# Optimization experiments

Hardware: AMD Instinct MI355X
Metric: run time of the kernel (lower is better)

The kernel has to match this reference:

```python
import jax, jax.numpy as jnp
import numpy as np

MAX_THRESHOLD = 0.25  # init kwarg
B, S, D, E = 8, 4096, 512, 8


def setup_inputs() -> dict:
    key = jax.random.key(0)
    ks = jax.random.split(key, 5)
    scale = 1.0 / np.sqrt(D)
    return {
        "inputs": jax.random.normal(ks[0], (B, S, D), dtype=jnp.float32),
        "W_gate": jax.random.normal(ks[1], (D, E), dtype=jnp.float32) * scale,
        "b_gate": jnp.zeros((E,), dtype=jnp.float32),
        "W_thr": jax.random.normal(ks[2], (D, 1), dtype=jnp.float32) * scale,
        "b_thr": jnp.zeros((1,), dtype=jnp.float32),
        "W_exp": jax.random.normal(ks[3], (E, D, D), dtype=jnp.float32) * scale,
        "b_exp": jnp.zeros((E, D), dtype=jnp.float32),
    }


def reference(inputs, W_gate, b_gate, W_thr, b_thr, W_exp, b_exp):
    d = inputs.shape[-1]
    x = inputs.reshape(-1, d)  # [T, D]
    # gating
    gate_logits = jax.nn.softmax(x @ W_gate + b_gate, axis=-1)          # [T, E]
    thresholds = jax.nn.sigmoid(x @ W_thr + b_thr) * MAX_THRESHOLD      # [T, 1]
    adapted = gate_logits - thresholds                                  # [T, E]
    selected = (adapted >= 0).astype(x.dtype)                           # [T, E]
    weights = adapted * selected                                        # [T, E]
    wsum = jnp.sum(weights, axis=-1, keepdims=True)
    wsum = jnp.where(wsum == 0, jnp.ones_like(wsum), wsum)
    weights = weights / wsum
    # dense-equivalent of gather->expert->scatter (weights are 0 where unselected)
    ex_out = jnp.einsum('td,edf->etf', x, W_exp) + b_exp[:, None, :]    # [E, T, D]
    results = jnp.einsum('etf,te->tf', ex_out, weights)                 # [T, D]
    return results.reshape(inputs.shape[:-1] + (results.shape[-1],))
```

## Files before the change

kernel.cpp:

```cpp
#include <hip/hip_runtime.h>


#define T_TOKENS 32768
#define DDIM 512
#define KDIM 4096
#define SLOTA 8192
#define SLOTB 16384

typedef __attribute__((ext_vector_type(8))) short short8;
typedef __attribute__((ext_vector_type(4))) float floatx4;
typedef __bf16 bf16x2 __attribute__((ext_vector_type(2)));

__device__ __forceinline__ unsigned short f2bf(float f) {
    unsigned int u = __float_as_uint(f);
    u += 0x7FFFu + ((u >> 16) & 1u);
    return (unsigned short)(u >> 16);
}

__device__ __forceinline__ unsigned int pk2(float a, float b) {
#if __has_builtin(__builtin_amdgcn_cvt_pk_bf16_f32)
    bf16x2 v = __builtin_amdgcn_cvt_pk_bf16_f32(a, b);
    return __builtin_bit_cast(unsigned int, v);
#else
    return (unsigned int)f2bf(a) | ((unsigned int)f2bf(b) << 16);
#endif
}

__device__ __forceinline__ void async_copy16(const void* g, void* l) {
    __builtin_amdgcn_global_load_lds(
        (const __attribute__((address_space(1))) void*)g,
        (__attribute__((address_space(3))) void*)l, 16, 0, 0);
}

__global__ __launch_bounds__(256) void gating_cvt(
    const float* __restrict__ x, const float* __restrict__ Wg,
    const float* __restrict__ bg, const float* __restrict__ Wt,
    const float* __restrict__ bt, float* __restrict__ wbuf,
    unsigned short* __restrict__ Xbf)
{
    __shared__ float sW[512 * 12];
    const int tid = threadIdx.x;
    for (int i = tid; i < 512 * 9; i += 256) {
        int d = i / 9, e = i - d * 9;
        sW[d * 12 + e] = (e < 8) ? Wg[d * 8 + e] : Wt[d];
    }
    __syncthreads();

    const int t = blockIdx.x * 64 + (tid >> 2);
    const int q = tid & 3;
    float g[9];
#pragma unroll
    for (int e = 0; e < 9; ++e) g[e] = 0.f;

    const float4* xr = (const float4*)(x + (size_t)t * 512 + q * 128);
    for (int i = 0; i < 32; ++i) {
        float4 v = xr[i];
        float xv[4] = {v.x, v.y, v.z, v.w};
        const float* wp = &sW[(q * 128 + i * 4) * 12];
#pragma unroll
        for (int c = 0; c < 4; ++c) {
            const float* w = wp + c * 12;
#pragma unroll
            for (int e = 0; e < 9; ++e) g[e] = fmaf(xv[c], w[e], g[e]);
        }
    }
#pragma unroll
    for (int e = 0; e < 9; ++e) {
        g[e] += __shfl_xor(g[e], 1);
        g[e] += __shfl_xor(g[e], 2);
    }
    if (q == 0) {
#pragma unroll
        for (int e = 0; e < 8; ++e) g[e] += bg[e];
        g[8] += bt[0];
        float m = g[0];
#pragma unroll
        for (int e = 1; e < 8; ++e) m = fmaxf(m, g[e]);
        float s = 0.f;
        float p[8];
#pragma unroll
        for (int e = 0; e < 8; ++e) { p[e] = __expf(g[e] - m); s += p[e]; }
        const float inv = 1.f / s;
        const float thr = 0.25f / (1.f + __expf(-g[8]));
        float w8[8];
        float ws = 0.f;
#pragma unroll
        for (int e = 0; e < 8; ++e) {
            float a = p[e] * inv - thr;
            w8[e] = a > 0.f ? a : 0.f;
            ws += w8[e];
        }
        if (ws == 0.f) ws = 1.f;
        const float invw = 1.f / ws;
        float4 o0, o1;
        o0.x = w8[0] * invw; o0.y = w8[1] * invw; o0.z = w8[2] * invw; o0.w = w8[3] * invw;
        o1.x = w8[4] * invw; o1.y = w8[5] * invw; o1.z = w8[6] * invw; o1.w = w8[7] * invw;
        float4* op = (float4*)(wbuf + (size_t)t * 8);
        op[0] = o0;
        op[1] = o1;
    }

    const size_t base = (size_t)blockIdx.x * 64 * 512;
    const float4* xs = (const float4*)(x + base);
    uint2* xd = (uint2*)(Xbf + base);
#pragma unroll 4
    for (int it = 0; it < 32; ++it) {
        float4 v = xs[it * 256 + tid];
        uint2 pk;
        pk.x = pk2(v.x, v.y);
        pk.y = pk2(v.z, v.w);
        xd[it * 256 + tid] = pk;
    }
}

__global__ __launch_bounds__(256) void build_bt(
    const float* __restrict__ Wexp, unsigned short* __restrict__ Bt)
{
    __shared__ float tile[64][65];
    const int k0 = blockIdx.x * 64;
    const int n0 = blockIdx.y * 64;
    const int tid = threadIdx.x;
    const int r = tid >> 4, cq = tid & 15;
#pragma unroll
    for (int p = 0; p < 4; ++p) {
        const int rr = p * 16 + r;
        const float4 v = *(const float4*)(Wexp + (size_t)(k0 + rr) * 512 + n0 + cq * 4);
        tile[rr][cq * 4 + 0] = v.x;
        tile[rr][cq * 4 + 1] = v.y;
        tile[rr][cq * 4 + 2] = v.z;
        tile[rr][cq * 4 + 3] = v.w;
    }
    __syncthreads();
    const int rn = tid >> 2;
    const int kq = tid & 3;
    alignas(16) unsigned short buf[16];
#pragma unroll
    for (int j = 0; j < 16; ++j) buf[j] = f2bf(tile[kq * 16 + j][rn]);
    unsigned short* dst = Bt + (size_t)(n0 + rn) * KDIM + k0 + kq * 16;
    *(uint4*)(dst) = *(const uint4*)(buf);
    *(uint4*)(dst + 8) = *(const uint4*)(buf + 8);
}

__global__ __launch_bounds__(512, 2) void moe_gemm(
    const unsigned short* __restrict__ Xbf, const float* __restrict__ wbuf,
    const float* __restrict__ bexp, const unsigned short* __restrict__ Bt,
    float* __restrict__ out)
{
    __shared__ alignas(16) unsigned short As[3 * 128 * 64];
    __shared__ alignas(16) unsigned short Bs[3 * 256 * 64];
    __shared__ float sWbT[8 * 128];

    const int tid = threadIdx.x;
    const int wave = tid >> 6;
    const int lane = tid & 63;
    const int wm = wave >> 2;
    const int wn = wave & 3;
    const int lm = lane & 15;
    const int lq = lane >> 4;
    const int brow = lane >> 3;
    const int cg = (lane & 7) ^ brow;

    const int lin = blockIdx.x;
    const int g = lin & 7;
    const int j_ = lin >> 3;
    const int t0 = (g * 32 + (j_ >> 1)) * 128;
    const int n0 = (j_ & 1) * 256;

    {
        const int row = tid & 127, q = tid >> 7;
        const float2 w2 = *(const float2*)(wbuf + (size_t)(t0 + row) * 8 + q * 2);
        sWbT[(q * 2 + 0) * 128 + row] = w2.x;
        sWbT[(q * 2 + 1) * 128 + row] = w2.y;
    }

#define STAGE(s_, slot_)                                                        \
    {                                                                           \
        const int d0_ = ((s_) & 7) << 6;                                        \
        _Pragma("unroll")                                                       \
        for (int i = 0; i < 2; ++i)                                             \
            async_copy16(Xbf + (size_t)(t0 + wave * 16 + i * 8 + brow) * 512 + d0_ + cg * 8, \
                         As + (slot_) * SLOTA + (wave * 16 + i * 8) * 64);      \
        const int k0_ = (s_) << 6;                                              \
        _Pragma("unroll")                                                       \
        for (int i = 0; i < 4; ++i)                                             \
            async_copy16(Bt + (size_t)(n0 + wave * 32 + i * 8 + brow) * KDIM + k0_ + cg * 8, \
                         Bs + (slot_) * SLOTB + (wave * 32 + i * 8) * 64);      \
    }

    STAGE(0, 0);
    STAGE(1, 1);
    __syncthreads();

    floatx4 acc[4][4], tmp[4][4];
#pragma unroll
    for (int i = 0; i < 4; ++i)
#pragma unroll
        for (int j = 0; j < 4; ++j) {
            acc[i][j] = (floatx4){0.f, 0.f, 0.f, 0.f};
            tmp[i][j] = (floatx4){0.f, 0.f, 0.f, 0.f};
        }

    int sl = 0;
    for (int s = 0; s < 64; ++s) {
        if (s < 62) {
            const int sl2 = (sl >= 1) ? sl - 1 : 2;
            STAGE(s + 2, sl2);
        }
        const unsigned short* Ab = As + sl * SLOTA;
        const unsigned short* Bb = Bs + sl * SLOTB;
        __builtin_amdgcn_s_setprio(1);
#pragma unroll
        for (int kk = 0; kk < 2; ++kk) {
            const int ch = kk * 4 + lq;
            short8 a[4], b[4];
#pragma unroll
            for (int i = 0; i < 4; ++i) {
                const int row = wm * 64 + i * 16 + lm;
                a[i] = *(const short8*)(Ab + row * 64 + ((ch ^ (row & 7)) << 3));
            }
#pragma unroll
            for (int j = 0; j < 4; ++j) {
                const int row = wn * 64 + j * 16 + lm;
                b[j] = *(const short8*)(Bb + row * 64 + ((ch ^ (row & 7)) << 3));
            }
#pragma unroll
            for (int i = 0; i < 4; ++i)
#pragma unroll
                for (int j = 0; j < 4; ++j)
                    tmp[i][j] = __builtin_amdgcn_mfma_f32_16x16x32_bf16(
                        a[i], b[j], tmp[i][j], 0, 0, 0);
        }
        __builtin_amdgcn_s_setprio(0);
        if ((s & 7) == 7) {
            const int e = s >> 3;
#pragma unroll
            for (int i = 0; i < 4; ++i) {
                const float4 wq = *(const float4*)(sWbT + e * 128 + wm * 64 + i * 16 + lq * 4);
#pragma unroll
                for (int j = 0; j < 4; ++j) {
                    acc[i][j][0] = fmaf(wq.x, tmp[i][j][0], acc[i][j][0]);
                    acc[i][j][1] = fmaf(wq.y, tmp[i][j][1], acc[i][j][1]);
                    acc[i][j][2] = fmaf(wq.z, tmp[i][j][2], acc[i][j][2]);
                    acc[i][j][3] = fmaf(wq.w, tmp[i][j][3], acc[i][j][3]);
                    tmp[i][j] = (floatx4){0.f, 0.f, 0.f, 0.f};
                }
            }
        }
        if (s < 62) {
            asm volatile("s_waitcnt vmcnt(6)" ::: "memory");
        } else if (s == 62) {
            asm volatile("s_waitcnt vmcnt(0)" ::: "memory");
        }
        if (s < 63) __builtin_amdgcn_s_barrier();
        sl = (sl >= 2) ? 0 : sl + 1;
    }

    float bc[4][8];
#pragma unroll
    for (int j = 0; j < 4; ++j) {
        const int col = n0 + wn * 64 + j * 16 + lm;
#pragma unroll
        for (int e = 0; e < 8; ++e) bc[j][e] = bexp[e * 512 + col];
    }
#pragma unroll
    for (int i = 0; i < 4; ++i)
#pragma unroll
        for (int r = 0; r < 4; ++r) {
            const int rowl = wm * 64 + i * 16 + lq * 4 + r;
            const float4 w0 = *(const float4*)(wbuf + (size_t)(t0 + rowl) * 8);
            const float4 w1 = *(const float4*)(wbuf + (size_t)(t0 + rowl) * 8 + 4);
            float* op = out + (size_t)(t0 + rowl) * 512 + n0 + wn * 64 + lm;
#pragma unroll
            for (int j = 0; j < 4; ++j) {
                float bias = w0.x * bc[j][0];
                bias = fmaf(w0.y, bc[j][1], bias);
                bias = fmaf(w0.z, bc[j][2], bias);
                bias = fmaf(w0.w, bc[j][3], bias);
                bias = fmaf(w1.x, bc[j][4], bias);
                bias = fmaf(w1.y, bc[j][5], bias);
                bias = fmaf(w1.z, bc[j][6], bias);
                bias = fmaf(w1.w, bc[j][7], bias);
                op[j * 16] = acc[i][j][r] + bias;
            }
        }
#undef STAGE
}

extern "C" void kernel_launch(void* const* d_in, const int* in_sizes, int n_in,
                              void* d_out, int out_size, void* d_ws, size_t ws_size,
                              hipStream_t stream) {
    const float* x   = (const float*)d_in[0];
    const float* Wg  = (const float*)d_in[1];
    const float* bg  = (const float*)d_in[2];
    const float* Wt  = (const float*)d_in[3];
    const float* bt  = (const float*)d_in[4];
    const float* Wex = (const float*)d_in[5];
    const float* bex = (const float*)d_in[6];
    float* out = (float*)d_out;

    unsigned short* Xbf = (unsigned short*)d_ws;
    unsigned short* Bt  = (unsigned short*)((char*)d_ws + (size_t)T_TOKENS * DDIM * 2);
    float* wbuf = (float*)((char*)d_ws + (size_t)T_TOKENS * DDIM * 2
                                       + (size_t)DDIM * KDIM * 2);

    gating_cvt<<<T_TOKENS / 64, 256, 0, stream>>>(x, Wg, bg, Wt, bt, wbuf, Xbf);
    build_bt<<<dim3(KDIM / 64, DDIM / 64), 256, 0, stream>>>(Wex, Bt);
    moe_gemm<<<512, 512, 0, stream>>>(Xbf, wbuf, bex, Bt, out);
}
```

Measured before the change: 322.1 us.

## Interleave async global loads with LDS reads and MFMA in two half-steps

Splits each K-step into two halves. Each half reads its A/B fragments from LDS, then issues part of the async prefetch for stage s+2 (A plus half of B first, the rest of B second), then runs the MFMA block between extra barriers. The goal is to spread global-load issue across the compute and keep waves in lockstep so memory and MFMA overlap better. It adds two more block-wide barriers per iteration, which may cost synchronisation stalls.

```diff
diff --git a/kernel.cpp b/kernel.cpp
--- a/kernel.cpp
+++ b/kernel.cpp
@@ -146,8 +146,8 @@
     const float* __restrict__ bexp, const unsigned short* __restrict__ Bt,
     float* __restrict__ out)
 {
-    __shared__ alignas(16) unsigned short As[3 * 128 * 64];
-    __shared__ alignas(16) unsigned short Bs[3 * 256 * 64];
+    __shared__ alignas(16) unsigned short As[3 * SLOTA];
+    __shared__ alignas(16) unsigned short Bs[3 * SLOTB];
     __shared__ float sWbT[8 * 128];
 
     const int tid = threadIdx.x;
@@ -173,22 +173,27 @@
         sWbT[(q * 2 + 1) * 128 + row] = w2.y;
     }
 
-#define STAGE(s_, slot_)                                                        \
+#define STAGE_A(s_, slot_)                                                      \
     {                                                                           \
         const int d0_ = ((s_) & 7) << 6;                                        \
         _Pragma("unroll")                                                       \
         for (int i = 0; i < 2; ++i)                                             \
             async_copy16(Xbf + (size_t)(t0 + wave * 16 + i * 8 + brow) * 512 + d0_ + cg * 8, \
                          As + (slot_) * SLOTA + (wave * 16 + i * 8) * 64);      \
+    }
+#define STAGE_B(s_, slot_, i0, i1)                                              \
+    {                                                                           \
         const int k0_ = (s_) << 6;                                              \
         _Pragma("unroll")                                                       \
-        for (int i = 0; i < 4; ++i)                                             \
+        for (int i = (i0); i < (i1); ++i)                                       \
             async_copy16(Bt + (size_t)(n0 + wave * 32 + i * 8 + brow) * KDIM + k0_ + cg * 8, \
                          Bs + (slot_) * SLOTB + (wave * 32 + i * 8) * 64);      \
     }
 
-    STAGE(0, 0);
-    STAGE(1, 1);
+    STAGE_A(0, 0);
+    STAGE_B(0, 0, 0, 4);
+    STAGE_A(1, 1);
+    STAGE_B(1, 1, 0, 4);
     __syncthreads();
 
     floatx4 acc[4][4], tmp[4][4];
@@ -202,17 +207,14 @@
 
     int sl = 0;
     for (int s = 0; s < 64; ++s) {
-        if (s < 62) {
-            const int sl2 = (sl >= 1) ? sl - 1 : 2;
-            STAGE(s + 2, sl2);
-        }
+        const int sl1 = (sl == 2) ? 0 : sl + 1;
+        const int sl2 = (sl == 0) ? 2 : sl - 1;
         const unsigned short* Ab = As + sl * SLOTA;
         const unsigned short* Bb = Bs + sl * SLOTB;
-        __builtin_amdgcn_s_setprio(1);
-#pragma unroll
-        for (int kk = 0; kk < 2; ++kk) {
-            const int ch = kk * 4 + lq;
+
+        {
             short8 a[4], b[4];
+            const int ch = lq;
 #pragma unroll
             for (int i = 0; i < 4; ++i) {
                 const int row = wm * 64 + i * 16 + lm;
@@ -223,14 +225,49 @@
                 const int row = wn * 64 + j * 16 + lm;
                 b[j] = *(const short8*)(Bb + row * 64 + ((ch ^ (row & 7)) << 3));
             }
+            if (s < 62) {
+                STAGE_A(s + 2, sl2);
+                STAGE_B(s + 2, sl2, 0, 2);
+            }
+            __builtin_amdgcn_s_barrier();
+            __builtin_amdgcn_s_setprio(1);
 #pragma unroll
             for (int i = 0; i < 4; ++i)
 #pragma unroll
                 for (int j = 0; j < 4; ++j)
                     tmp[i][j] = __builtin_amdgcn_mfma_f32_16x16x32_bf16(
                         a[i], b[j], tmp[i][j], 0, 0, 0);
-        }
-        __builtin_amdgcn_s_setprio(0);
+            __builtin_amdgcn_s_setprio(0);
+            __builtin_amdgcn_s_barrier();
+        }
+
+        {
+            short8 a[4], b[4];
+            const int ch = 4 + lq;
+#pragma unroll
+            for (int i = 0; i < 4; ++i) {
+                const int row = wm * 64 + i * 16 + lm;
+                a[i] = *(const short8*)(Ab + row * 64 + ((ch ^ (row & 7)) << 3));
+            }
+#pragma unroll
+            for (int j = 0; j < 4; ++j) {
+                const int row = wn * 64 + j * 16 + lm;
+                b[j] = *(const short8*)(Bb + row * 64 + ((ch ^ (row & 7)) << 3));
+            }
+            if (s < 62) {
+                STAGE_B(s + 2, sl2, 2, 4);
+            }
+            __builtin_amdgcn_s_barrier();
+            __builtin_amdgcn_s_setprio(1);
+#pragma unroll
+            for (int i = 0; i < 4; ++i)
+#pragma unroll
+                for (int j = 0; j < 4; ++j)
+                    tmp[i][j] = __builtin_amdgcn_mfma_f32_16x16x32_bf16(
+                        a[i], b[j], tmp[i][j], 0, 0, 0);
+            __builtin_amdgcn_s_setprio(0);
+        }
+
         if ((s & 7) == 7) {
             const int e = s >> 3;
 #pragma unroll
@@ -246,13 +283,14 @@
                 }
             }
         }
+
         if (s < 62) {
             asm volatile("s_waitcnt vmcnt(6)" ::: "memory");
         } else if (s == 62) {
             asm volatile("s_waitcnt vmcnt(0)" ::: "memory");
         }
-        if (s < 63) __builtin_amdgcn_s_barrier();
-        sl = (sl >= 2) ? 0 : sl + 1;
+        __builtin_amdgcn_s_barrier();
+        sl = sl1;
     }
 
     float bc[4][8];
@@ -283,7 +321,8 @@
                 op[j * 16] = acc[i][j][r] + bias;
             }
         }
-#undef STAGE
+#undef STAGE_A
+#undef STAGE_B
 }
 
 extern "C" void kernel_launch(void* const* d_in, const int* in_sizes, int n_in,
```

Measured after the change: 290.1 us. 1.11x faster.

## Pre-scale A by gate weights, enlarge token tile, fuse weight transpose into gating

Applied to the files above, without the earlier changes.

The gating kernel and the expert-weight transpose/convert kernel are merged into one launch, removing a kernel launch. The GEMM now loads X through registers, multiplies each row by its per-expert gate weight, and writes the scaled bf16 tile to LDS. This lets MFMAs accumulate straight into one accumulator and drops the tmp accumulators and periodic FMA reduction. The token tile doubles to 256 rows (256 blocks), A is single-buffered, and the k-step is split into quarter phases with many barriers. In exchange it adds an extra bf16 rounding of the scaled inputs, more register pressure, and a lot more barrier synchronisation.

```diff
diff --git a/kernel.cpp b/kernel.cpp
--- a/kernel.cpp
+++ b/kernel.cpp
@@ -4,8 +4,8 @@
 #define T_TOKENS 32768
 #define DDIM 512
 #define KDIM 4096
-#define SLOTA 8192
 #define SLOTB 16384
+#define SLOTA 16384
 
 typedef __attribute__((ext_vector_type(8))) short short8;
 typedef __attribute__((ext_vector_type(4))) float floatx4;
@@ -32,14 +32,49 @@
         (__attribute__((address_space(3))) void*)l, 16, 0, 0);
 }
 
-__global__ __launch_bounds__(256) void gating_cvt(
+__device__ __forceinline__ unsigned int scale_pair(unsigned int u, float w) {
+    float lo = __uint_as_float(u << 16) * w;
+    float hi = __uint_as_float(u & 0xFFFF0000u) * w;
+    return pk2(lo, hi);
+}
+
+__global__ __launch_bounds__(256) void gating_cvt_bt(
     const float* __restrict__ x, const float* __restrict__ Wg,
     const float* __restrict__ bg, const float* __restrict__ Wt,
     const float* __restrict__ bt, float* __restrict__ wbuf,
-    unsigned short* __restrict__ Xbf)
+    unsigned short* __restrict__ Xbf,
+    const float* __restrict__ Wexp, unsigned short* __restrict__ Bt)
 {
     __shared__ float sW[512 * 12];
     const int tid = threadIdx.x;
+
+    if (blockIdx.x >= 512) {
+        float(*tile)[65] = (float(*)[65])sW;
+        const int bb = blockIdx.x - 512;
+        const int k0 = (bb & 63) * 64;
+        const int n0 = (bb >> 6) * 64;
+        const int r = tid >> 4, cq = tid & 15;
+#pragma unroll
+        for (int p = 0; p < 4; ++p) {
+            const int rr = p * 16 + r;
+            const float4 v = *(const float4*)(Wexp + (size_t)(k0 + rr) * 512 + n0 + cq * 4);
+            tile[rr][cq * 4 + 0] = v.x;
+            tile[rr][cq * 4 + 1] = v.y;
+            tile[rr][cq * 4 + 2] = v.z;
+            tile[rr][cq * 4 + 3] = v.w;
+        }
+        __syncthreads();
+        const int rn = tid >> 2;
+        const int kq = tid & 3;
+        alignas(16) unsigned short buf[16];
+#pragma unroll
+        for (int j = 0; j < 16; ++j) buf[j] = f2bf(tile[kq * 16 + j][rn]);
+        unsigned short* dst = Bt + (size_t)(n0 + rn) * KDIM + k0 + kq * 16;
+        *(uint4*)(dst) = *(const uint4*)(buf);
+        *(uint4*)(dst + 8) = *(const uint4*)(buf + 8);
+        return;
+    }
+
     for (int i = tid; i < 512 * 9; i += 256) {
         int d = i / 9, e = i - d * 9;
         sW[d * 12 + e] = (e < 8) ? Wg[d * 8 + e] : Wt[d];
@@ -113,42 +148,14 @@
     }
 }
 
-__global__ __launch_bounds__(256) void build_bt(
-    const float* __restrict__ Wexp, unsigned short* __restrict__ Bt)
-{
-    __shared__ float tile[64][65];
-    const int k0 = blockIdx.x * 64;
-    const int n0 = blockIdx.y * 64;
-    const int tid = threadIdx.x;
-    const int r = tid >> 4, cq = tid & 15;
-#pragma unroll
-    for (int p = 0; p < 4; ++p) {
-        const int rr = p * 16 + r;
-        const float4 v = *(const float4*)(Wexp + (size_t)(k0 + rr) * 512 + n0 + cq * 4);
-        tile[rr][cq * 4 + 0] = v.x;
-        tile[rr][cq * 4 + 1] = v.y;
-        tile[rr][cq * 4 + 2] = v.z;
-        tile[rr][cq * 4 + 3] = v.w;
-    }
-    __syncthreads();
-    const int rn = tid >> 2;
-    const int kq = tid & 3;
-    alignas(16) unsigned short buf[16];
-#pragma unroll
-    for (int j = 0; j < 16; ++j) buf[j] = f2bf(tile[kq * 16 + j][rn]);
-    unsigned short* dst = Bt + (size_t)(n0 + rn) * KDIM + k0 + kq * 16;
-    *(uint4*)(dst) = *(const uint4*)(buf);
-    *(uint4*)(dst + 8) = *(const uint4*)(buf + 8);
-}
-
 __global__ __launch_bounds__(512, 2) void moe_gemm(
     const unsigned short* __restrict__ Xbf, const float* __restrict__ wbuf,
     const float* __restrict__ bexp, const unsigned short* __restrict__ Bt,
     float* __restrict__ out)
 {
-    __shared__ alignas(16) unsigned short As[3 * 128 * 64];
-    __shared__ alignas(16) unsigned short Bs[3 * 256 * 64];
-    __shared__ float sWbT[8 * 128];
+    __shared__ alignas(16) unsigned short Bs[3 * SLOTB];
+    __shared__ alignas(16) unsigned short As[SLOTA];
+    __shared__ float sWbT[8 * 256];
 
     const int tid = threadIdx.x;
     const int wave = tid >> 6;
@@ -159,100 +166,146 @@
     const int lq = lane >> 4;
     const int brow = lane >> 3;
     const int cg = (lane & 7) ^ brow;
+    const int c8 = tid & 7;
+    const int r0 = tid >> 3;
+    const int swzA = ((c8 ^ (r0 & 7)) << 3);
 
     const int lin = blockIdx.x;
     const int g = lin & 7;
     const int j_ = lin >> 3;
-    const int t0 = (g * 32 + (j_ >> 1)) * 128;
+    const int t0 = (g * 16 + (j_ >> 1)) * 256;
     const int n0 = (j_ & 1) * 256;
 
     {
-        const int row = tid & 127, q = tid >> 7;
-        const float2 w2 = *(const float2*)(wbuf + (size_t)(t0 + row) * 8 + q * 2);
-        sWbT[(q * 2 + 0) * 128 + row] = w2.x;
-        sWbT[(q * 2 + 1) * 128 + row] = w2.y;
-    }
-
-#define STAGE(s_, slot_)                                                        \
-    {                                                                           \
-        const int d0_ = ((s_) & 7) << 6;                                        \
-        _Pragma("unroll")                                                       \
-        for (int i = 0; i < 2; ++i)                                             \
-            async_copy16(Xbf + (size_t)(t0 + wave * 16 + i * 8 + brow) * 512 + d0_ + cg * 8, \
-                         As + (slot_) * SLOTA + (wave * 16 + i * 8) * 64);      \
+        const int row = tid & 255, pr = tid >> 8;
+        const float4 w4 = *(const float4*)(wbuf + (size_t)(t0 + row) * 8 + pr * 4);
+        sWbT[(pr * 4 + 0) * 256 + row] = w4.x;
+        sWbT[(pr * 4 + 1) * 256 + row] = w4.y;
+        sWbT[(pr * 4 + 2) * 256 + row] = w4.z;
+        sWbT[(pr * 4 + 3) * 256 + row] = w4.w;
+    }
+
+#define STAGE_B(s_, slot_, i0, i1)                                              \
+    {                                                                           \
         const int k0_ = (s_) << 6;                                              \
         _Pragma("unroll")                                                       \
-        for (int i = 0; i < 4; ++i)                                             \
+        for (int i = (i0); i < (i1); ++i)                                       \
             async_copy16(Bt + (size_t)(n0 + wave * 32 + i * 8 + brow) * KDIM + k0_ + cg * 8, \
                          Bs + (slot_) * SLOTB + (wave * 32 + i * 8) * 64);      \
     }
-
-    STAGE(0, 0);
-    STAGE(1, 1);
-    __syncthreads();
-
-    floatx4 acc[4][4], tmp[4][4];
-#pragma unroll
-    for (int i = 0; i < 4; ++i)
-#pragma unroll
-        for (int j = 0; j < 4; ++j) {
-            acc[i][j] = (floatx4){0.f, 0.f, 0.f, 0.f};
-            tmp[i][j] = (floatx4){0.f, 0.f, 0.f, 0.f};
-        }
-
-    int sl = 0;
+#define LOADA_ISSUE(s_)                                                         \
+    {                                                                           \
+        const int d0_ = ((s_) & 7) << 6;                                        \
+        _Pragma("unroll")                                                       \
+        for (int m = 0; m < 4; ++m)                                             \
+            ar[m] = *(const uint4*)(Xbf + (size_t)(t0 + r0 + m * 64) * 512 + d0_ + c8 * 8); \
+    }
+#define ASCALE_WRITE(s_)                                                        \
+    {                                                                           \
+        const int e1 = (s_) >> 3;                                               \
+        _Pragma("unroll")                                                       \
+        for (int m = 0; m < 4; ++m) {                                           \
+            const float w = sWbT[e1 * 256 + r0 + m * 64];                       \
+            uint4 o;                                                            \
+            o.x = scale_pair(ar[m].x, w);                                       \
+            o.y = scale_pair(ar[m].y, w);                                       \
+            o.z = scale_pair(ar[m].z, w);                                       \
+            o.w = scale_pair(ar[m].w, w);                                       \
+            *(uint4*)(As + (r0 + m * 64) * 64 + swzA) = o;                      \
+        }                                                                       \
+    }
+#define READ_A(ih)                                                              \
+    {                                                                           \
+        _Pragma("unroll")                                                       \
+        for (int ii = 0; ii < 4; ++ii)                                          \
+            _Pragma("unroll")                                                   \
+            for (int kk = 0; kk < 2; ++kk) {                                    \
+                const int row = wm * 128 + ((ih) * 4 + ii) * 16 + lm;           \
+                const int ch = kk * 4 + lq;                                     \
+                af[ii][kk] = *(const short8*)(As + row * 64 + ((ch ^ (row & 7)) << 3)); \
+            }                                                                   \
+    }
+#define READ_B(q_, dst)                                                         \
+    {                                                                           \
+        _Pragma("unroll")                                                       \
+        for (int jj = 0; jj < 2; ++jj)                                          \
+            _Pragma("unroll")                                                   \
+            for (int kk = 0; kk < 2; ++kk) {                                    \
+                const int row = wn * 64 + ((q_) * 2 + jj) * 16 + lm;            \
+                const int ch = kk * 4 + lq;                                     \
+                dst[jj][kk] = *(const short8*)(Bb + row * 64 + ((ch ^ (row & 7)) << 3)); \
+            }                                                                   \
+    }
+#define MFMA_Q(ih, q_, bq)                                                      \
+    {                                                                           \
+        __builtin_amdgcn_s_setprio(1);                                          \
+        _Pragma("unroll")                                                       \
+        for (int ii = 0; ii < 4; ++ii)                                          \
+            _Pragma("unroll")                                                   \
+            for (int jj = 0; jj < 2; ++jj)                                      \
+                _Pragma("unroll")                                               \
+                for (int kk = 0; kk < 2; ++kk)                                  \
+                    acc[(ih) * 4 + ii][(q_) * 2 + jj] =                         \
+                        __builtin_amdgcn_mfma_f32_16x16x32_bf16(                \
+                            af[ii][kk], bq[jj][kk], acc[(ih) * 4 + ii][(q_) * 2 + jj], 0, 0, 0); \
+        __builtin_amdgcn_s_setprio(0);                                          \
+    }
+
+    floatx4 acc[8][4];
+#pragma unroll
+    for (int i = 0; i < 8; ++i)
+#pragma unroll
+        for (int j = 0; j < 4; ++j) acc[i][j] = (floatx4){0.f, 0.f, 0.f, 0.f};
+
+    uint4 ar[4];
+
+    LOADA_ISSUE(0);
+    STAGE_B(0, 0, 0, 4);
+    STAGE_B(1, 1, 0, 4);
+    asm volatile("s_waitcnt vmcnt(8)" ::: "memory");
+    ASCALE_WRITE(0);
+    asm volatile("s_waitcnt vmcnt(4) lgkmcnt(0)" ::: "memory");
+    __builtin_amdgcn_s_barrier();
+
+    int sB = 0;
     for (int s = 0; s < 64; ++s) {
+        const int sB1 = (sB == 2) ? 0 : sB + 1;
+        const int sB2 = (sB == 0) ? 2 : sB - 1;
+        const unsigned short* Bb = Bs + sB * SLOTB;
+        short8 af[4][2], b0[2][2], b1[2][2];
+
+        READ_A(0);
+        READ_B(0, b0);
+        if (s < 63) LOADA_ISSUE(s + 1);
+        __builtin_amdgcn_s_barrier();
+        MFMA_Q(0, 0, b0);
+        __builtin_amdgcn_s_barrier();
+
+        READ_B(1, b1);
+        if (s < 62) STAGE_B(s + 2, sB2, 0, 2);
+        __builtin_amdgcn_s_barrier();
+        MFMA_Q(0, 1, b1);
+        __builtin_amdgcn_s_barrier();
+
+        READ_A(1);
+        if (s < 62) STAGE_B(s + 2, sB2, 2, 4);
+        __builtin_amdgcn_s_barrier();
+        MFMA_Q(1, 1, b1);
+        __builtin_amdgcn_s_barrier();
+
         if (s < 62) {
-            const int sl2 = (sl >= 1) ? sl - 1 : 2;
-            STAGE(s + 2, sl2);
-        }
-        const unsigned short* Ab = As + sl * SLOTA;
-        const unsigned short* Bb = Bs + sl * SLOTB;
-        __builtin_amdgcn_s_setprio(1);
-#pragma unroll
-        for (int kk = 0; kk < 2; ++kk) {
-            const int ch = kk * 4 + lq;
-            short8 a[4], b[4];
-#pragma unroll
-            for (int i = 0; i < 4; ++i) {
-                const int row = wm * 64 + i * 16 + lm;
-                a[i] = *(const short8*)(Ab + row * 64 + ((ch ^ (row & 7)) << 3));
-            }
-#pragma unroll
-            for (int j = 0; j < 4; ++j) {
-                const int row = wn * 64 + j * 16 + lm;
-                b[j] = *(const short8*)(Bb + row * 64 + ((ch ^ (row & 7)) << 3));
-            }
-#pragma unroll
-            for (int i = 0; i < 4; ++i)
-#pragma unroll
-                for (int j = 0; j < 4; ++j)
-                    tmp[i][j] = __builtin_amdgcn_mfma_f32_16x16x32_bf16(
-                        a[i], b[j], tmp[i][j], 0, 0, 0);
-        }
-        __builtin_amdgcn_s_setprio(0);
-        if ((s & 7) == 7) {
-            const int e = s >> 3;
-#pragma unroll
-            for (int i = 0; i < 4; ++i) {
-                const float4 wq = *(const float4*)(sWbT + e * 128 + wm * 64 + i * 16 + lq * 4);
-#pragma unroll
-                for (int j = 0; j < 4; ++j) {
-                    acc[i][j][0] = fmaf(wq.x, tmp[i][j][0], acc[i][j][0]);
-                    acc[i][j][1] = fmaf(wq.y, tmp[i][j][1], acc[i][j][1]);
-                    acc[i][j][2] = fmaf(wq.z, tmp[i][j][2], acc[i][j][2]);
-                    acc[i][j][3] = fmaf(wq.w, tmp[i][j][3], acc[i][j][3]);
-                    tmp[i][j] = (floatx4){0.f, 0.f, 0.f, 0.f};
-                }
-            }
-        }
-        if (s < 62) {
-            asm volatile("s_waitcnt vmcnt(6)" ::: "memory");
+            asm volatile("s_waitcnt vmcnt(4)" ::: "memory");
         } else if (s == 62) {
             asm volatile("s_waitcnt vmcnt(0)" ::: "memory");
         }
-        if (s < 63) __builtin_amdgcn_s_barrier();
-        sl = (sl >= 2) ? 0 : sl + 1;
+        if (s < 63) ASCALE_WRITE(s + 1);
+        READ_B(0, b0);
+        __builtin_amdgcn_s_barrier();
+        MFMA_Q(1, 0, b0);
+        asm volatile("s_waitcnt lgkmcnt(0)" ::: "memory");
+        __builtin_amdgcn_s_barrier();
+
+        sB = sB1;
     }
 
     float bc[4][8];
@@ -263,10 +316,10 @@
         for (int e = 0; e < 8; ++e) bc[j][e] = bexp[e * 512 + col];
     }
 #pragma unroll
-    for (int i = 0; i < 4; ++i)
+    for (int i = 0; i < 8; ++i)
 #pragma unroll
         for (int r = 0; r < 4; ++r) {
-            const int rowl = wm * 64 + i * 16 + lq * 4 + r;
+            const int rowl = wm * 128 + i * 16 + lq * 4 + r;
             const float4 w0 = *(const float4*)(wbuf + (size_t)(t0 + rowl) * 8);
             const float4 w1 = *(const float4*)(wbuf + (size_t)(t0 + rowl) * 8 + 4);
             float* op = out + (size_t)(t0 + rowl) * 512 + n0 + wn * 64 + lm;
@@ -283,7 +336,12 @@
                 op[j * 16] = acc[i][j][r] + bias;
             }
         }
-#undef STAGE
+#undef STAGE_B
+#undef LOADA_ISSUE
+#undef ASCALE_WRITE
+#undef READ_A
+#undef READ_B
+#undef MFMA_Q
 }
 
 extern "C" void kernel_launch(void* const* d_in, const int* in_sizes, int n_in,
@@ -303,7 +361,6 @@
     float* wbuf = (float*)((char*)d_ws + (size_t)T_TOKENS * DDIM * 2
                                        + (size_t)DDIM * KDIM * 2);
 
-    gating_cvt<<<T_TOKENS / 64, 256, 0, stream>>>(x, Wg, bg, Wt, bt, wbuf, Xbf);
-    build_bt<<<dim3(KDIM / 64, DDIM / 64), 256, 0, stream>>>(Wex, Bt);
-    moe_gemm<<<512, 512, 0, stream>>>(Xbf, wbuf, bex, Bt, out);
-}
+    gating_cvt_bt<<<1024, 256, 0, stream>>>(x, Wg, bg, Wt, bt, wbuf, Xbf, Wex, Bt);
+    moe_gemm<<<256, 512, 0, stream>>>(Xbf, wbuf, bex, Bt, out);
+}
```

Result: faster. 286.7 us (-11.0%).
